# Optimization experiments

Measured on AMD Instinct MI355X. Metric: run time of the kernel, lower is better.

## Reference

```python
import jax, jax.numpy as jnp
import numpy as np


def setup_inputs() -> dict:
    key = jax.random.key(0)
    ks = jax.random.split(key, 7)
    B, S, E, H, D = 4, 2048, 1024, 16, 64
    return {
        "q": jax.random.normal(ks[0], (B, S, E), dtype=jnp.float32),
        "k": jax.random.normal(ks[1], (B, S, E), dtype=jnp.float32),
        "v": jax.random.normal(ks[2], (B, S, E), dtype=jnp.float32),
        "Wq": jax.random.uniform(ks[3], (H, E, D), dtype=jnp.float32),
        "Wk": jax.random.uniform(ks[4], (H, E, D), dtype=jnp.float32),
        "Wv": jax.random.uniform(ks[5], (H, E, D), dtype=jnp.float32),
        "Wo": jax.random.uniform(ks[6], (H * D, E), dtype=jnp.float32),
    }


def reference(q, k, v, Wq, Wk, Wv, Wo):
    B, S, E = q.shape
    H, _, D = Wq.shape
    qh = jnp.einsum("bse,hed->bhsd", q, Wq)
    kh = jnp.einsum("bse,hed->bhsd", k, Wk)
    vh = jnp.einsum("bse,hed->bhsd", v, Wv)
    # Faithful quirk: original divides by C**(-0.5) -> multiplies by sqrt(D)
    scale = jnp.asarray(D, q.dtype) ** 0.5
    scores = jnp.einsum("bhsd,bhtd->bhst", qh, kh) * scale  # [B,H,S,S]
    causal = jnp.tril(jnp.ones((S, S), dtype=bool))
    scores = jnp.where(causal, scores, -jnp.inf)
    attn = jax.nn.softmax(scores, axis=-1)
    out_h = jnp.einsum("bhst,bhtd->bhsd", attn, vh)  # [B,H,S,D]
    concat = out_h.transpose(0, 2, 1, 3).reshape(B, S, H * D)
    return concat @ Wo
```

## Files before the change

### kernel.cpp

```cpp
#include <hip/hip_runtime.h>
#include <hip/hip_bf16.h>

#define B_ 4
#define S_ 2048
#define E_ 1024
#define H_ 16
#define D_ 64

typedef _Float16 f16;
typedef __attribute__((ext_vector_type(4))) float f32x4;
typedef __attribute__((ext_vector_type(8))) short bf16x8;
typedef __attribute__((ext_vector_type(8))) unsigned short u16x8;
typedef __attribute__((ext_vector_type(8))) _Float16 f16x8;
typedef __attribute__((ext_vector_type(4))) float float4v;

__device__ __forceinline__ unsigned short f2bf(float f) {
  union { float f; unsigned int u; } x; x.f = f;
  unsigned int u = x.u;
  u = (u + 0x7FFFu + ((u >> 16) & 1u)) >> 16;
  return (unsigned short)u;
}

#define MFMA_BF(a, b, c) __builtin_amdgcn_mfma_f32_16x16x32_bf16((a), (b), (c), 0, 0, 0)
#define MFMA_F16(a, b, c) __builtin_amdgcn_mfma_f32_16x16x32_f16((a), (b), (c), 0, 0, 0)

#define GLDS16(g, s) __builtin_amdgcn_global_load_lds( \
    (const __attribute__((address_space(1))) void*)(g), \
    (__attribute__((address_space(3))) void*)(s), 16, 0, 0)

__global__ __launch_bounds__(256)
void transpose_convert(const float* __restrict__ src, unsigned short* __restrict__ dst,
                       int R, int C, float scale) {
  __shared__ unsigned short tile[64][65];
  const int rb = blockIdx.y * 64;
  const int cb = blockIdx.x * 64;
  const size_t mo = (size_t)blockIdx.z * (size_t)R * (size_t)C;
  const int t = threadIdx.x;
  const int r = t >> 2;
  const int c0 = (t & 3) * 16;
  const float* sp = src + mo + (size_t)(rb + r) * C + cb + c0;
#pragma unroll
  for (int j = 0; j < 16; j += 4) {
    float4v vv = *(const float4v*)(sp + j);
    tile[r][c0 + j + 0] = f2bf(vv[0] * scale);
    tile[r][c0 + j + 1] = f2bf(vv[1] * scale);
    tile[r][c0 + j + 2] = f2bf(vv[2] * scale);
    tile[r][c0 + j + 3] = f2bf(vv[3] * scale);
  }
  __syncthreads();
  u16x8 w0, w1;
#pragma unroll
  for (int j = 0; j < 8; ++j) w0[j] = tile[c0 + j][r];
#pragma unroll
  for (int j = 0; j < 8; ++j) w1[j] = tile[c0 + 8 + j][r];
  unsigned short* dp = dst + mo + (size_t)(cb + r) * R + rb + c0;
  *(u16x8*)(dp) = w0;
  *(u16x8*)(dp + 8) = w1;
}

__global__ __launch_bounds__(256)
void transpose_split_f16(const float* __restrict__ src, f16* __restrict__ dhi,
                         f16* __restrict__ dlo, int R, int C, float scale) {
  __shared__ float tile[64][65];
  const int rb = blockIdx.y * 64;
  const int cb = blockIdx.x * 64;
  const size_t mo = (size_t)blockIdx.z * (size_t)R * (size_t)C;
  const int t = threadIdx.x;
  const int r = t >> 2;
  const int c0 = (t & 3) * 16;
  const float* sp = src + mo + (size_t)(rb + r) * C + cb + c0;
#pragma unroll
  for (int j = 0; j < 16; j += 4) {
    float4v vv = *(const float4v*)(sp + j);
    tile[r][c0 + j + 0] = vv[0] * scale;
    tile[r][c0 + j + 1] = vv[1] * scale;
    tile[r][c0 + j + 2] = vv[2] * scale;
    tile[r][c0 + j + 3] = vv[3] * scale;
  }
  __syncthreads();
  f16x8 h0, h1, l0, l1;
#pragma unroll
  for (int j = 0; j < 8; ++j) {
    float x = tile[c0 + j][r];
    f16 hi = (f16)x;
    h0[j] = hi; l0[j] = (f16)(x - (float)hi);
  }
#pragma unroll
  for (int j = 0; j < 8; ++j) {
    float x = tile[c0 + 8 + j][r];
    f16 hi = (f16)x;
    h1[j] = hi; l1[j] = (f16)(x - (float)hi);
  }
  const size_t o = mo + (size_t)(cb + r) * R + rb + c0;
  *(f16x8*)(dhi + o) = h0; *(f16x8*)(dhi + o + 8) = h1;
  *(f16x8*)(dlo + o) = l0; *(f16x8*)(dlo + o + 8) = l1;
}

__global__ __launch_bounds__(256)
void prep_split(const float* __restrict__ x, f16* __restrict__ xh, f16* __restrict__ xl) {
  const size_t i = ((size_t)blockIdx.x * 256 + threadIdx.x) * 8;
  float4v a = *(const float4v*)(x + i);
  float4v b = *(const float4v*)(x + i + 4);
  f16x8 h, lo;
#pragma unroll
  for (int j = 0; j < 4; ++j) {
    f16 hi = (f16)a[j]; h[j] = hi; lo[j] = (f16)(a[j] - (float)hi);
  }
#pragma unroll
  for (int j = 0; j < 4; ++j) {
    f16 hi = (f16)b[j]; h[4 + j] = hi; lo[4 + j] = (f16)(b[j] - (float)hi);
  }
  *(f16x8*)(xh + i) = h;
  *(f16x8*)(xl + i) = lo;
}

__global__ __launch_bounds__(256)
void prep_bf16(const float* __restrict__ x, unsigned short* __restrict__ xo) {
  const size_t i = ((size_t)blockIdx.x * 256 + threadIdx.x) * 8;
  float4v a = *(const float4v*)(x + i);
  float4v b = *(const float4v*)(x + i + 4);
  u16x8 o;
#pragma unroll
  for (int j = 0; j < 4; ++j) { o[j] = f2bf(a[j]); o[4 + j] = f2bf(b[j]); }
  *(u16x8*)(xo + i) = o;
}

__global__ __launch_bounds__(256, 2)
void proj_qk3(const f16* __restrict__ xh, const f16* __restrict__ xl,
              const f16* __restrict__ Wh, const f16* __restrict__ Wl,
              f16* __restrict__ out_hi, f16* __restrict__ out_lo) {
  __shared__ f16 Ah[128 * 32], Al[128 * 32], Bh[128 * 32], Bl[128 * 32];
  const int t = threadIdx.x;
  const int m0 = blockIdx.x * 128, n0 = blockIdx.y * 128;
  const int w = t >> 6, l = t & 63, lr = l & 15, lg = l >> 4;
  const int wm = (w & 1) * 64, wn = (w >> 1) * 64;
  const int srow = w * 32 + (l >> 2);
  const int scol = (l & 3) * 8;

  f32x4 acc[4][4];
#pragma unroll
  for (int im = 0; im < 4; ++im)
#pragma unroll
    for (int in = 0; in < 4; ++in) acc[im][in] = (f32x4){0.f, 0.f, 0.f, 0.f};

  for (int k0 = 0; k0 < 1024; k0 += 32) {
#pragma unroll
    for (int j = 0; j < 2; ++j) {
      const size_t ga = (size_t)(m0 + srow + j * 16) * 1024 + scol + k0;
      const size_t gb = (size_t)(n0 + srow + j * 16) * 1024 + scol + k0;
      const int lo = (w * 32 + j * 16) * 32;
      GLDS16(xh + ga, &Ah[lo]);
      GLDS16(xl + ga, &Al[lo]);
      GLDS16(Wh + gb, &Bh[lo]);
      GLDS16(Wl + gb, &Bl[lo]);
    }
    __syncthreads();

    f16x8 afh[4], afl[4], bfh[4], bfl[4];
#pragma unroll
    for (int im = 0; im < 4; ++im) {
      afh[im] = *(const f16x8*)&Ah[(wm + im * 16 + lr) * 32 + lg * 8];
      afl[im] = *(const f16x8*)&Al[(wm + im * 16 + lr) * 32 + lg * 8];
    }
#pragma unroll
    for (int in = 0; in < 4; ++in) {
      bfh[in] = *(const f16x8*)&Bh[(wn + in * 16 + lr) * 32 + lg * 8];
      bfl[in] = *(const f16x8*)&Bl[(wn + in * 16 + lr) * 32 + lg * 8];
    }
#pragma unroll
    for (int im = 0; im < 4; ++im)
#pragma unroll
      for (int in = 0; in < 4; ++in) {
        acc[im][in] = MFMA_F16(afh[im], bfh[in], acc[im][in]);
        acc[im][in] = MFMA_F16(afh[im], bfl[in], acc[im][in]);
        acc[im][in] = MFMA_F16(afl[im], bfh[in], acc[im][in]);
      }
    __syncthreads();
  }

  const int b = m0 >> 11, s0b = m0 & 2047;
#pragma unroll
  for (int im = 0; im < 4; ++im)
#pragma unroll
    for (int in = 0; in < 4; ++in)
#pragma unroll
      for (int rr = 0; rr < 4; ++rr) {
        const int srw = s0b + wm + im * 16 + lg * 4 + rr;
        const int n = n0 + wn + in * 16 + lr;
        const int h = n >> 6, d = n & 63;
        const size_t o = (((size_t)b * H_ + h) * S_ + srw) * D_ + d;
        const float x = acc[im][in][rr];
        const f16 hi = (f16)x;
        out_hi[o] = hi;
        out_lo[o] = (f16)(x - (float)hi);
      }
}

__global__ __launch_bounds__(256, 2)
void proj_v3(const unsigned short* __restrict__ xv, const unsigned short* __restrict__ Wv,
             f16* __restrict__ vht) {
  __shared__ short smem[17408];
  unsigned short* As = (unsigned short*)smem;
  unsigned short* Bs = As + 128 * 32;
  const int t = threadIdx.x;
  const int m0 = blockIdx.x * 128, n0 = blockIdx.y * 128;
  const int w = t >> 6, l = t & 63, lr = l & 15, lg = l >> 4;
  const int wm = (w & 1) * 64, wn = (w >> 1) * 64;
  const int srow = w * 32 + (l >> 2);
  const int scol = (l & 3) * 8;

  f32x4 acc[4][4];
#pragma unroll
  for (int im = 0; im < 4; ++im)
#pragma unroll
    for (int in = 0; in < 4; ++in) acc[im][in] = (f32x4){0.f, 0.f, 0.f, 0.f};

  for (int k0 = 0; k0 < 1024; k0 += 32) {
#pragma unroll
    for (int j = 0; j < 2; ++j) {
      const size_t ga = (size_t)(m0 + srow + j * 16) * 1024 + scol + k0;
      const size_t gb = (size_t)(n0 + srow + j * 16) * 1024 + scol + k0;
      const int lo = (w * 32 + j * 16) * 32;
      GLDS16(xv + ga, &As[lo]);
      GLDS16(Wv + gb, &Bs[lo]);
    }
    __syncthreads();

    bf16x8 af[4], bf[4];
#pragma unroll
    for (int im = 0; im < 4; ++im)
      af[im] = *(const bf16x8*)&As[(wm + im * 16 + lr) * 32 + lg * 8];
#pragma unroll
    for (int in = 0; in < 4; ++in)
      bf[in] = *(const bf16x8*)&Bs[(wn + in * 16 + lr) * 32 + lg * 8];
#pragma unroll
    for (int im = 0; im < 4; ++im)
#pragma unroll
      for (int in = 0; in < 4; ++in)
        acc[im][in] = MFMA_BF(af[im], bf[in], acc[im][in]);
    __syncthreads();
  }

  f16* Td = (f16*)smem;
#pragma unroll
  for (int im = 0; im < 4; ++im)
#pragma unroll
    for (int in = 0; in < 4; ++in)
#pragma unroll
      for (int rr = 0; rr < 4; ++rr) {
        const int srw = wm + im * 16 + lg * 4 + rr;
        const int ncol = wn + in * 16 + lr;
        Td[ncol * 136 + srw] = (f16)acc[im][in][rr];
      }
  __syncthreads();
  const int n = t >> 1, sc2 = (t & 1) * 64;
  const int b = m0 >> 11, s0b = m0 & 2047;
  const int h = (n0 + n) >> 6, d = (n0 + n) & 63;
  f16* vp = vht + (((size_t)b * H_ + h) * D_ + d) * S_ + s0b + sc2;
#pragma unroll
  for (int j = 0; j < 8; ++j)
    *(f16x8*)(vp + j * 8) = *(const f16x8*)&Td[n * 136 + sc2 + j * 8];
}

__global__ __launch_bounds__(256, 2)
void out_gemm3(const unsigned short* __restrict__ A, const unsigned short* __restrict__ Bt,
               float* __restrict__ Cout) {
  __shared__ unsigned short As[128 * 32], Bs[128 * 32];
  const int t = threadIdx.x;
  const int m0 = blockIdx.x * 128, n0 = blockIdx.y * 128;
  const int w = t >> 6, l = t & 63, lr = l & 15, lg = l >> 4;
  const int wm = (w & 1) * 64, wn = (w >> 1) * 64;
  const int srow = w * 32 + (l >> 2);
  const int scol = (l & 3) * 8;

  f32x4 acc[4][4];
#pragma unroll
  for (int im = 0; im < 4; ++im)
#pragma unroll
    for (int in = 0; in < 4; ++in) acc[im][in] = (f32x4){0.f, 0.f, 0.f, 0.f};

  for (int k0 = 0; k0 < 1024; k0 += 32) {
#pragma unroll
    for (int j = 0; j < 2; ++j) {
      const size_t ga = (size_t)(m0 + srow + j * 16) * 1024 + scol + k0;
      const size_t gb = (size_t)(n0 + srow + j * 16) * 1024 + scol + k0;
      const int lo = (w * 32 + j * 16) * 32;
      GLDS16(A + ga, &As[lo]);
      GLDS16(Bt + gb, &Bs[lo]);
    }
    __syncthreads();

    bf16x8 af[4], bf[4];
#pragma unroll
    for (int im = 0; im < 4; ++im)
      af[im] = *(const bf16x8*)&As[(wm + im * 16 + lr) * 32 + lg * 8];
#pragma unroll
    for (int in = 0; in < 4; ++in)
      bf[in] = *(const bf16x8*)&Bs[(wn + in * 16 + lr) * 32 + lg * 8];
#pragma unroll
    for (int im = 0; im < 4; ++im)
#pragma unroll
      for (int in = 0; in < 4; ++in)
        acc[im][in] = MFMA_BF(af[im], bf[in], acc[im][in]);
    __syncthreads();
  }

#pragma unroll
  for (int im = 0; im < 4; ++im)
#pragma unroll
    for (int in = 0; in < 4; ++in)
#pragma unroll
      for (int rr = 0; rr < 4; ++rr) {
        const int row = m0 + wm + im * 16 + lg * 4 + rr;
        const int col = n0 + wn + in * 16 + lr;
        Cout[(size_t)row * 1024 + col] = acc[im][in][rr];
      }
}

__global__ __launch_bounds__(256, 2)
void attn_kernel(const f16* __restrict__ qhh, const f16* __restrict__ qhl,
                 const f16* __restrict__ khh, const f16* __restrict__ khl,
                 const f16* __restrict__ vht, unsigned short* __restrict__ ao) {
  __shared__ f16 Ksh[2][64 * 64];
  __shared__ f16 Ksl[2][64 * 64];
  __shared__ f16 Vts[2][64 * 64];
  __shared__ f16 Pls[4][32 * 64];
  const int t = threadIdx.x;
  const int b = blockIdx.z, h = blockIdx.y;
  const int w = t >> 6, l = t & 63, lr = l & 15, lg = l >> 4;
  const size_t bh = ((size_t)b * H_ + h) * S_;
  const size_t bhD = ((size_t)b * H_ + h) * D_;
  const int cr0 = t >> 3, cch = t & 7;
  const int cr1 = (t + 256) >> 3;
  const int coff = (cch * 16);

#pragma unroll
  for (int ph = 0; ph < 2; ++ph) {
    const int qt = ph ? (15 - (int)blockIdx.x) : (int)blockIdx.x;
    const int q0 = qt * 128;

    f16x8 qfh[2][2], qfl[2][2];
#pragma unroll
    for (int i = 0; i < 2; ++i) {
      const size_t qo = (bh + q0 + w * 32 + i * 16 + lr) * D_;
#pragma unroll
      for (int hf = 0; hf < 2; ++hf) {
        qfh[i][hf] = *(const f16x8*)(qhh + qo + hf * 32 + lg * 8);
        qfl[i][hf] = *(const f16x8*)(qhl + qo + hf * 32 + lg * 8);
      }
    }

    f32x4 acc[2][4];
#pragma unroll
    for (int i = 0; i < 2; ++i)
#pragma unroll
      for (int c = 0; c < 4; ++c) acc[i][c] = (f32x4){0.f, 0.f, 0.f, 0.f};
    float mx[2][4], ls[2][4];
#pragma unroll
    for (int i = 0; i < 2; ++i)
#pragma unroll
      for (int r = 0; r < 4; ++r) { mx[i][r] = -3.0e38f; ls[i][r] = 0.f; }

    const int wmax = q0 + w * 32 + 31;
    const int nkt = 2 * qt + 2;
    int cur = 0;

    {
      const f16* kbh = khh + bh * D_;
      const f16* kbl = khl + bh * D_;
      const f16* vb = vht + bhD * S_;
      f16x8 a0 = *(const f16x8*)(kbh + cr0 * 64 + cch * 8);
      f16x8 a1 = *(const f16x8*)(kbh + cr1 * 64 + cch * 8);
      f16x8 b0 = *(const f16x8*)(kbl + cr0 * 64 + cch * 8);
      f16x8 b1 = *(const f16x8*)(kbl + cr1 * 64 + cch * 8);
      f16x8 c0 = *(const f16x8*)(vb + (size_t)cr0 * S_ + cch * 8);
      f16x8 c1 = *(const f16x8*)(vb + (size_t)cr1 * S_ + cch * 8);
      const int o0 = coff ^ ((cr0 & 7) << 4);
      const int o1 = coff ^ ((cr1 & 7) << 4);
      *(f16x8*)((char*)Ksh[0] + cr0 * 128 + o0) = a0;
      *(f16x8*)((char*)Ksh[0] + cr1 * 128 + o1) = a1;
      *(f16x8*)((char*)Ksl[0] + cr0 * 128 + o0) = b0;
      *(f16x8*)((char*)Ksl[0] + cr1 * 128 + o1) = b1;
      *(f16x8*)((char*)Vts[0] + cr0 * 128 + o0) = c0;
      *(f16x8*)((char*)Vts[0] + cr1 * 128 + o1) = c1;
    }

    for (int kt = 0; kt < nkt; ++kt) {
      const int kt0 = kt * 64;
      __syncthreads();

      const bool pf = (kt + 1 < nkt);
      f16x8 ra0, ra1, rb0, rb1, rc0, rc1;
      if (pf) {
        const int n0 = kt0 + 64;
        const f16* kbh = khh + (bh + n0) * D_;
        const f16* kbl = khl + (bh + n0) * D_;
        const f16* vb = vht + bhD * S_ + n0;
        ra0 = *(const f16x8*)(kbh + cr0 * 64 + cch * 8);
        ra1 = *(const f16x8*)(kbh + cr1 * 64 + cch * 8);
        rb0 = *(const f16x8*)(kbl + cr0 * 64 + cch * 8);
        rb1 = *(const f16x8*)(kbl + cr1 * 64 + cch * 8);
        rc0 = *(const f16x8*)(vb + (size_t)cr0 * S_ + cch * 8);
        rc1 = *(const f16x8*)(vb + (size_t)cr1 * S_ + cch * 8);
      }

      if (kt0 <= wmax) {
        f32x4 sc[2][4];
#pragma unroll
        for (int n = 0; n < 4; ++n) {
          const int krow = n * 16 + lr;
          const int sw = (krow & 7) << 4;
          const char* kb = (const char*)Ksh[cur] + krow * 128;
          const char* kbl2 = (const char*)Ksl[cur] + krow * 128;
          f16x8 kh0 = *(const f16x8*)(kb + ((lg * 16) ^ sw));
          f16x8 kh1 = *(const f16x8*)(kb + ((64 + lg * 16) ^ sw));
          f16x8 kl0 = *(const f16x8*)(kbl2 + ((lg * 16) ^ sw));
          f16x8 kl1 = *(const f16x8*)(kbl2 + ((64 + lg * 16) ^ sw));
#pragma unroll
          for (int i = 0; i < 2; ++i) {
            f32x4 z = (f32x4){0.f, 0.f, 0.f, 0.f};
            z = MFMA_F16(qfh[i][0], kh0, z);
            z = MFMA_F16(qfh[i][1], kh1, z);
            z = MFMA_F16(qfh[i][0], kl0, z);
            z = MFMA_F16(qfh[i][1], kl1, z);
            z = MFMA_F16(qfl[i][0], kh0, z);
            z = MFMA_F16(qfl[i][1], kh1, z);
            sc[i][n] = z;
          }
        }

#pragma unroll
        for (int i = 0; i < 2; ++i) {
          const int qbase = q0 + w * 32 + i * 16;
          const bool full = (kt0 + 63 <= qbase);
#pragma unroll
          for (int r = 0; r < 4; ++r) {
            const int qrow = qbase + lg * 4 + r;
            float v0 = sc[i][0][r], v1 = sc[i][1][r], v2 = sc[i][2][r], v3 = sc[i][3][r];
            if (!full) {
              v0 = (kt0 + 0 + lr <= qrow) ? v0 : -3.0e38f;
              v1 = (kt0 + 16 + lr <= qrow) ? v1 : -3.0e38f;
              v2 = (kt0 + 32 + lr <= qrow) ? v2 : -3.0e38f;
              v3 = (kt0 + 48 + lr <= qrow) ? v3 : -3.0e38f;
            }
            float tm = fmaxf(fmaxf(v0, v1), fmaxf(v2, v3));
            tm = fmaxf(tm, __shfl_xor(tm, 1));
            tm = fmaxf(tm, __shfl_xor(tm, 2));
            tm = fmaxf(tm, __shfl_xor(tm, 4));
            tm = fmaxf(tm, __shfl_xor(tm, 8));
            const float mn = fmaxf(mx[i][r], tm);
            const float corr = __expf(mx[i][r] - mn);
            mx[i][r] = mn;
            float p0 = __expf(v0 - mn), p1 = __expf(v1 - mn);
            float p2 = __expf(v2 - mn), p3 = __expf(v3 - mn);
            float ps = (p0 + p1) + (p2 + p3);
            ps += __shfl_xor(ps, 1);
            ps += __shfl_xor(ps, 2);
            ps += __shfl_xor(ps, 4);
            ps += __shfl_xor(ps, 8);
            ls[i][r] = ls[i][r] * corr + ps;
#pragma unroll
            for (int c = 0; c < 4; ++c) acc[i][c][r] *= corr;
            const int qi = i * 16 + lg * 4 + r;
            char* pb = (char*)&Pls[w][0] + qi * 128;
            const int sw2 = (qi & 7) << 4;
            *(f16*)(pb + ((0 + lr * 2) ^ sw2)) = (f16)p0;
            *(f16*)(pb + ((32 + lr * 2) ^ sw2)) = (f16)p1;
            *(f16*)(pb + ((64 + lr * 2) ^ sw2)) = (f16)p2;
            *(f16*)(pb + ((96 + lr * 2) ^ sw2)) = (f16)p3;
          }
        }

#pragma unroll
        for (int ks = 0; ks < 2; ++ks) {
          const int co = (ks * 64 + lg * 16);
          f16x8 pf0 = *(const f16x8*)((const char*)&Pls[w][0] + lr * 128 + (co ^ ((lr & 7) << 4)));
          f16x8 pf1 = *(const f16x8*)((const char*)&Pls[w][0] + (16 + lr) * 128 + (co ^ ((lr & 7) << 4)));
#pragma unroll
          for (int c = 0; c < 4; ++c) {
            const int vr = c * 16 + lr;
            f16x8 vf = *(const f16x8*)((const char*)Vts[cur] + vr * 128 + (co ^ ((vr & 7) << 4)));
            acc[0][c] = MFMA_F16(pf0, vf, acc[0][c]);
            acc[1][c] = MFMA_F16(pf1, vf, acc[1][c]);
          }
        }
      }

      __syncthreads();
      if (pf) {
        const int nb = cur ^ 1;
        const int o0 = coff ^ ((cr0 & 7) << 4);
        const int o1 = coff ^ ((cr1 & 7) << 4);
        *(f16x8*)((char*)Ksh[nb] + cr0 * 128 + o0) = ra0;
        *(f16x8*)((char*)Ksh[nb] + cr1 * 128 + o1) = ra1;
        *(f16x8*)((char*)Ksl[nb] + cr0 * 128 + o0) = rb0;
        *(f16x8*)((char*)Ksl[nb] + cr1 * 128 + o1) = rb1;
        *(f16x8*)((char*)Vts[nb] + cr0 * 128 + o0) = rc0;
        *(f16x8*)((char*)Vts[nb] + cr1 * 128 + o1) = rc1;
      }
      cur ^= 1;
    }

#pragma unroll
    for (int i = 0; i < 2; ++i)
#pragma unroll
      for (int r = 0; r < 4; ++r) {
        const float inv = 1.0f / ls[i][r];
        const size_t s = q0 + w * 32 + i * 16 + lg * 4 + r;
        const size_t o = ((size_t)b * S_ + s) * (H_ * D_) + (size_t)h * D_;
#pragma unroll
        for (int c = 0; c < 4; ++c)
          ao[o + c * 16 + lr] = f2bf(acc[i][c][r] * inv);
      }
  }
}

extern "C" void kernel_launch(void* const* d_in, const int* in_sizes, int n_in,
                              void* d_out, int out_size, void* d_ws, size_t ws_size,
                              hipStream_t stream) {
  const float* q = (const float*)d_in[0];
  const float* k = (const float*)d_in[1];
  const float* v = (const float*)d_in[2];
  const float* Wq = (const float*)d_in[3];
  const float* Wk = (const float*)d_in[4];
  const float* Wv = (const float*)d_in[5];
  const float* Wo = (const float*)d_in[6];

  const size_t NBH = (size_t)B_ * H_ * S_ * D_;
  const size_t WSZ = (size_t)H_ * D_ * E_;

  char* wsb = (char*)d_ws;
  f16* Wqk_hi = (f16*)wsb;
  f16* Wqk_lo = Wqk_hi + 2 * WSZ;
  unsigned short* Wvt = (unsigned short*)(Wqk_lo + 2 * WSZ);
  unsigned short* Wot = Wvt + WSZ;
  f16* qk_hi = (f16*)(wsb + (size_t)12 * 1024 * 1024);
  f16* qk_lo = qk_hi + 2 * NBH;
  char* flex = wsb + (size_t)76 * 1024 * 1024;
  f16* xh = (f16*)flex;
  f16* xl = (f16*)(flex + (size_t)16 * 1024 * 1024);
  unsigned short* xv = (unsigned short*)flex;
  f16* vht = (f16*)(flex + (size_t)16 * 1024 * 1024);
  unsigned short* ao = (unsigned short*)flex;

  dim3 blk(256);
  transpose_split_f16<<<dim3(1, 16, 16), blk, 0, stream>>>(Wq, Wqk_hi, Wqk_lo, E_, D_, 8.0f);
  transpose_split_f16<<<dim3(1, 16, 16), blk, 0, stream>>>(Wk, Wqk_hi + WSZ, Wqk_lo + WSZ, E_, D_, 1.0f);
  transpose_convert<<<dim3(1, 16, 16), blk, 0, stream>>>(Wv, Wvt, E_, D_, 1.0f);
  transpose_convert<<<dim3(16, 16, 1), blk, 0, stream>>>(Wo, Wot, E_, E_, 1.0f);
  prep_split<<<dim3(4096), blk, 0, stream>>>(q, xh, xl);
  proj_qk3<<<dim3(64, 8), blk, 0, stream>>>(xh, xl, Wqk_hi, Wqk_lo, qk_hi, qk_lo);
  prep_split<<<dim3(4096), blk, 0, stream>>>(k, xh, xl);
  proj_qk3<<<dim3(64, 8), blk, 0, stream>>>(xh, xl, Wqk_hi + WSZ, Wqk_lo + WSZ,
                                            qk_hi + NBH, qk_lo + NBH);
  prep_bf16<<<dim3(4096), blk, 0, stream>>>(v, xv);
  proj_v3<<<dim3(64, 8), blk, 0, stream>>>(xv, Wvt, vht);
  attn_kernel<<<dim3(S_ / 256, H_, B_), blk, 0, stream>>>(
      qk_hi, qk_lo, qk_hi + NBH, qk_lo + NBH, vht, ao);
  out_gemm3<<<dim3(64, 8), blk, 0, stream>>>(ao, Wot, (float*)d_out);
}
```

Baseline: 485.9 us.

## Double GEMM K-tile to 64, add MFMA priority hints, skip redundant softmax rescale

The three projection/output GEMM kernels now stage 64-wide K tiles in shared memory instead of 32, which halves the number of barrier-separated iterations and doubles LDS use per block. The attention kernel wraps its MFMA sections in s_setprio to favor matrix issue across waves. It also skips the accumulator rescale when no row max in the wave changed, using a wave-wide vote. The larger LDS footprint may reduce occupancy, and the vote adds a branch.

```diff
diff --git a/kernel.cpp b/kernel.cpp
--- a/kernel.cpp
+++ b/kernel.cpp
@@ -129,13 +129,13 @@
 void proj_qk3(const f16* __restrict__ xh, const f16* __restrict__ xl,
               const f16* __restrict__ Wh, const f16* __restrict__ Wl,
               f16* __restrict__ out_hi, f16* __restrict__ out_lo) {
-  __shared__ f16 Ah[128 * 32], Al[128 * 32], Bh[128 * 32], Bl[128 * 32];
+  __shared__ f16 Ah[128 * 64], Al[128 * 64], Bh[128 * 64], Bl[128 * 64];
   const int t = threadIdx.x;
   const int m0 = blockIdx.x * 128, n0 = blockIdx.y * 128;
   const int w = t >> 6, l = t & 63, lr = l & 15, lg = l >> 4;
   const int wm = (w & 1) * 64, wn = (w >> 1) * 64;
-  const int srow = w * 32 + (l >> 2);
-  const int scol = (l & 3) * 8;
+  const int srow = l >> 3;
+  const int scol = (l & 7) * 8;
 
   f32x4 acc[4][4];
 #pragma unroll
@@ -143,12 +143,13 @@
 #pragma unroll
     for (int in = 0; in < 4; ++in) acc[im][in] = (f32x4){0.f, 0.f, 0.f, 0.f};
 
-  for (int k0 = 0; k0 < 1024; k0 += 32) {
-#pragma unroll
-    for (int j = 0; j < 2; ++j) {
-      const size_t ga = (size_t)(m0 + srow + j * 16) * 1024 + scol + k0;
-      const size_t gb = (size_t)(n0 + srow + j * 16) * 1024 + scol + k0;
-      const int lo = (w * 32 + j * 16) * 32;
+  for (int k0 = 0; k0 < 1024; k0 += 64) {
+#pragma unroll
+    for (int j = 0; j < 4; ++j) {
+      const int ch = w * 4 + j;
+      const size_t ga = (size_t)(m0 + ch * 8 + srow) * 1024 + k0 + scol;
+      const size_t gb = (size_t)(n0 + ch * 8 + srow) * 1024 + k0 + scol;
+      const int lo = ch * 512;
       GLDS16(xh + ga, &Ah[lo]);
       GLDS16(xl + ga, &Al[lo]);
       GLDS16(Wh + gb, &Bh[lo]);
@@ -156,25 +157,28 @@
     }
     __syncthreads();
 
-    f16x8 afh[4], afl[4], bfh[4], bfl[4];
-#pragma unroll
-    for (int im = 0; im < 4; ++im) {
-      afh[im] = *(const f16x8*)&Ah[(wm + im * 16 + lr) * 32 + lg * 8];
-      afl[im] = *(const f16x8*)&Al[(wm + im * 16 + lr) * 32 + lg * 8];
-    }
-#pragma unroll
-    for (int in = 0; in < 4; ++in) {
-      bfh[in] = *(const f16x8*)&Bh[(wn + in * 16 + lr) * 32 + lg * 8];
-      bfl[in] = *(const f16x8*)&Bl[(wn + in * 16 + lr) * 32 + lg * 8];
-    }
-#pragma unroll
-    for (int im = 0; im < 4; ++im)
+#pragma unroll
+    for (int hf = 0; hf < 2; ++hf) {
+      f16x8 afh[4], afl[4], bfh[4], bfl[4];
+#pragma unroll
+      for (int im = 0; im < 4; ++im) {
+        afh[im] = *(const f16x8*)&Ah[(wm + im * 16 + lr) * 64 + hf * 32 + lg * 8];
+        afl[im] = *(const f16x8*)&Al[(wm + im * 16 + lr) * 64 + hf * 32 + lg * 8];
+      }
 #pragma unroll
       for (int in = 0; in < 4; ++in) {
-        acc[im][in] = MFMA_F16(afh[im], bfh[in], acc[im][in]);
-        acc[im][in] = MFMA_F16(afh[im], bfl[in], acc[im][in]);
-        acc[im][in] = MFMA_F16(afl[im], bfh[in], acc[im][in]);
-      }
+        bfh[in] = *(const f16x8*)&Bh[(wn + in * 16 + lr) * 64 + hf * 32 + lg * 8];
+        bfl[in] = *(const f16x8*)&Bl[(wn + in * 16 + lr) * 64 + hf * 32 + lg * 8];
+      }
+#pragma unroll
+      for (int im = 0; im < 4; ++im)
+#pragma unroll
+        for (int in = 0; in < 4; ++in) {
+          acc[im][in] = MFMA_F16(afh[im], bfh[in], acc[im][in]);
+          acc[im][in] = MFMA_F16(afh[im], bfl[in], acc[im][in]);
+          acc[im][in] = MFMA_F16(afl[im], bfh[in], acc[im][in]);
+        }
+    }
     __syncthreads();
   }
 
@@ -201,13 +205,13 @@
              f16* __restrict__ vht) {
   __shared__ short smem[17408];
   unsigned short* As = (unsigned short*)smem;
-  unsigned short* Bs = As + 128 * 32;
+  unsigned short* Bs = As + 128 * 64;
   const int t = threadIdx.x;
   const int m0 = blockIdx.x * 128, n0 = blockIdx.y * 128;
   const int w = t >> 6, l = t & 63, lr = l & 15, lg = l >> 4;
   const int wm = (w & 1) * 64, wn = (w >> 1) * 64;
-  const int srow = w * 32 + (l >> 2);
-  const int scol = (l & 3) * 8;
+  const int srow = l >> 3;
+  const int scol = (l & 7) * 8;
 
   f32x4 acc[4][4];
 #pragma unroll
@@ -215,29 +219,33 @@
 #pragma unroll
     for (int in = 0; in < 4; ++in) acc[im][in] = (f32x4){0.f, 0.f, 0.f, 0.f};
 
-  for (int k0 = 0; k0 < 1024; k0 += 32) {
-#pragma unroll
-    for (int j = 0; j < 2; ++j) {
-      const size_t ga = (size_t)(m0 + srow + j * 16) * 1024 + scol + k0;
-      const size_t gb = (size_t)(n0 + srow + j * 16) * 1024 + scol + k0;
-      const int lo = (w * 32 + j * 16) * 32;
+  for (int k0 = 0; k0 < 1024; k0 += 64) {
+#pragma unroll
+    for (int j = 0; j < 4; ++j) {
+      const int ch = w * 4 + j;
+      const size_t ga = (size_t)(m0 + ch * 8 + srow) * 1024 + k0 + scol;
+      const size_t gb = (size_t)(n0 + ch * 8 + srow) * 1024 + k0 + scol;
+      const int lo = ch * 512;
       GLDS16(xv + ga, &As[lo]);
       GLDS16(Wv + gb, &Bs[lo]);
     }
     __syncthreads();
 
-    bf16x8 af[4], bf[4];
-#pragma unroll
-    for (int im = 0; im < 4; ++im)
-      af[im] = *(const bf16x8*)&As[(wm + im * 16 + lr) * 32 + lg * 8];
-#pragma unroll
-    for (int in = 0; in < 4; ++in)
-      bf[in] = *(const bf16x8*)&Bs[(wn + in * 16 + lr) * 32 + lg * 8];
-#pragma unroll
-    for (int im = 0; im < 4; ++im)
+#pragma unroll
+    for (int hf = 0; hf < 2; ++hf) {
+      bf16x8 af[4], bf[4];
+#pragma unroll
+      for (int im = 0; im < 4; ++im)
+        af[im] = *(const bf16x8*)&As[(wm + im * 16 + lr) * 64 + hf * 32 + lg * 8];
 #pragma unroll
       for (int in = 0; in < 4; ++in)
-        acc[im][in] = MFMA_BF(af[im], bf[in], acc[im][in]);
+        bf[in] = *(const bf16x8*)&Bs[(wn + in * 16 + lr) * 64 + hf * 32 + lg * 8];
+#pragma unroll
+      for (int im = 0; im < 4; ++im)
+#pragma unroll
+        for (int in = 0; in < 4; ++in)
+          acc[im][in] = MFMA_BF(af[im], bf[in], acc[im][in]);
+    }
     __syncthreads();
   }
 
@@ -265,13 +273,13 @@
 __global__ __launch_bounds__(256, 2)
 void out_gemm3(const unsigned short* __restrict__ A, const unsigned short* __restrict__ Bt,
                float* __restrict__ Cout) {
-  __shared__ unsigned short As[128 * 32], Bs[128 * 32];
+  __shared__ unsigned short As[128 * 64], Bs[128 * 64];
   const int t = threadIdx.x;
   const int m0 = blockIdx.x * 128, n0 = blockIdx.y * 128;
   const int w = t >> 6, l = t & 63, lr = l & 15, lg = l >> 4;
   const int wm = (w & 1) * 64, wn = (w >> 1) * 64;
-  const int srow = w * 32 + (l >> 2);
-  const int scol = (l & 3) * 8;
+  const int srow = l >> 3;
+  const int scol = (l & 7) * 8;
 
   f32x4 acc[4][4];
 #pragma unroll
@@ -279,29 +287,33 @@
 #pragma unroll
     for (int in = 0; in < 4; ++in) acc[im][in] = (f32x4){0.f, 0.f, 0.f, 0.f};
 
-  for (int k0 = 0; k0 < 1024; k0 += 32) {
-#pragma unroll
-    for (int j = 0; j < 2; ++j) {
-      const size_t ga = (size_t)(m0 + srow + j * 16) * 1024 + scol + k0;
-      const size_t gb = (size_t)(n0 + srow + j * 16) * 1024 + scol + k0;
-      const int lo = (w * 32 + j * 16) * 32;
+  for (int k0 = 0; k0 < 1024; k0 += 64) {
+#pragma unroll
+    for (int j = 0; j < 4; ++j) {
+      const int ch = w * 4 + j;
+      const size_t ga = (size_t)(m0 + ch * 8 + srow) * 1024 + k0 + scol;
+      const size_t gb = (size_t)(n0 + ch * 8 + srow) * 1024 + k0 + scol;
+      const int lo = ch * 512;
       GLDS16(A + ga, &As[lo]);
       GLDS16(Bt + gb, &Bs[lo]);
     }
     __syncthreads();
 
-    bf16x8 af[4], bf[4];
-#pragma unroll
-    for (int im = 0; im < 4; ++im)
-      af[im] = *(const bf16x8*)&As[(wm + im * 16 + lr) * 32 + lg * 8];
-#pragma unroll
-    for (int in = 0; in < 4; ++in)
-      bf[in] = *(const bf16x8*)&Bs[(wn + in * 16 + lr) * 32 + lg * 8];
-#pragma unroll
-    for (int im = 0; im < 4; ++im)
+#pragma unroll
+    for (int hf = 0; hf < 2; ++hf) {
+      bf16x8 af[4], bf[4];
+#pragma unroll
+      for (int im = 0; im < 4; ++im)
+        af[im] = *(const bf16x8*)&As[(wm + im * 16 + lr) * 64 + hf * 32 + lg * 8];
 #pragma unroll
       for (int in = 0; in < 4; ++in)
-        acc[im][in] = MFMA_BF(af[im], bf[in], acc[im][in]);
+        bf[in] = *(const bf16x8*)&Bs[(wn + in * 16 + lr) * 64 + hf * 32 + lg * 8];
+#pragma unroll
+      for (int im = 0; im < 4; ++im)
+#pragma unroll
+        for (int in = 0; in < 4; ++in)
+          acc[im][in] = MFMA_BF(af[im], bf[in], acc[im][in]);
+    }
     __syncthreads();
   }
 
@@ -406,6 +418,7 @@
 
       if (kt0 <= wmax) {
         f32x4 sc[2][4];
+        __builtin_amdgcn_s_setprio(1);
 #pragma unroll
         for (int n = 0; n < 4; ++n) {
           const int krow = n * 16 + lr;
@@ -428,6 +441,7 @@
             sc[i][n] = z;
           }
         }
+        __builtin_amdgcn_s_setprio(0);
 
 #pragma unroll
         for (int i = 0; i < 2; ++i) {
@@ -448,9 +462,8 @@
             tm = fmaxf(tm, __shfl_xor(tm, 2));
             tm = fmaxf(tm, __shfl_xor(tm, 4));
             tm = fmaxf(tm, __shfl_xor(tm, 8));
-            const float mn = fmaxf(mx[i][r], tm);
-            const float corr = __expf(mx[i][r] - mn);
-            mx[i][r] = mn;
+            const float mo = mx[i][r];
+            const float mn = fmaxf(mo, tm);
             float p0 = __expf(v0 - mn), p1 = __expf(v1 - mn);
             float p2 = __expf(v2 - mn), p3 = __expf(v3 - mn);
             float ps = (p0 + p1) + (p2 + p3);
@@ -458,9 +471,15 @@
             ps += __shfl_xor(ps, 2);
             ps += __shfl_xor(ps, 4);
             ps += __shfl_xor(ps, 8);
-            ls[i][r] = ls[i][r] * corr + ps;
-#pragma unroll
-            for (int c = 0; c < 4; ++c) acc[i][c][r] *= corr;
+            if (__all(mn == mo)) {
+              ls[i][r] += ps;
+            } else {
+              const float corr = __expf(mo - mn);
+              mx[i][r] = mn;
+              ls[i][r] = ls[i][r] * corr + ps;
+#pragma unroll
+              for (int c = 0; c < 4; ++c) acc[i][c][r] *= corr;
+            }
             const int qi = i * 16 + lg * 4 + r;
             char* pb = (char*)&Pls[w][0] + qi * 128;
             const int sw2 = (qi & 7) << 4;
@@ -471,6 +490,7 @@
           }
         }
 
+        __builtin_amdgcn_s_setprio(1);
 #pragma unroll
         for (int ks = 0; ks < 2; ++ks) {
           const int co = (ks * 64 + lg * 16);
@@ -484,6 +504,7 @@
             acc[1][c] = MFMA_F16(pf1, vf, acc[1][c]);
           }
         }
+        __builtin_amdgcn_s_setprio(0);
       }
 
       __syncthreads();
```

After: 499.2 us. 2.7% more time.
